# Performance work log

Measured on AMD Instinct MI355X. Metric: run time of the kernel, lower is better.

The kernel has to match this reference:

```python
import jax, jax.numpy as jnp
import numpy as np

P_DIM, L_DIM, D, O = 1100, 1024, 1024, 1024  # protein/label embed dims, latent, mlp width
B, NL = 16, 5000  # num_sequences, num_labels


def setup_inputs() -> dict:
    key = jax.random.key(0)
    ks = jax.random.split(key, 10)
    s = 0.02
    return {
        "sequence_embeddings": jax.random.normal(ks[0], (B, P_DIM), jnp.float32),
        "label_embeddings": jax.random.normal(ks[1], (NL, L_DIM), jnp.float32),
        "Wp": jax.random.normal(ks[2], (D, P_DIM), jnp.float32) * s,  # W_p (no bias)
        "Wl": jax.random.normal(ks[3], (D, L_DIM), jnp.float32) * s,  # W_l (no bias)
        "W1": jax.random.normal(ks[4], (O, 2 * D), jnp.float32) * s,  # Linear(2D -> O)
        "b1": jnp.zeros((O,), jnp.float32),
        "W2": jax.random.normal(ks[5], (O, O), jnp.float32) * s,      # Linear(O -> O)
        "b2": jnp.zeros((O,), jnp.float32),
        "W3": jax.random.normal(ks[6], (1, O), jnp.float32) * s,      # Linear(O -> 1)
        "b3": jnp.zeros((1,), jnp.float32),
    }


def reference(sequence_embeddings, label_embeddings, Wp, Wl, W1, b1, W2, b2, W3, b3):
    # Latent projections
    P_e = sequence_embeddings @ Wp.T           # [B, D]
    L_e = label_embeddings @ Wl.T              # [NL, D]
    # First MLP layer on concat([P_e, L_e]) over the cross join, computed by
    # splitting W1 into its P and L halves and broadcast-summing (same math as
    # cat + Linear, avoids materializing the [B*NL, 2D] concat).
    hp = P_e @ W1[:, :D].T                     # [B, O]
    hl = L_e @ W1[:, D:].T                     # [NL, O]
    h = jax.nn.relu(hp[:, None, :] + hl[None, :, :] + b1)   # [B, NL, O]
    h = jax.nn.relu(h @ W2.T + b2)             # [B, NL, O]
    logits = (h @ W3.T + b3)[..., 0]           # [B, NL]
    return logits
```

## Files before the change

### kernel.cpp

```cpp
#include <hip/hip_runtime.h>
#include <hip/hip_bf16.h>
#include <stdint.h>

typedef __bf16 bf16;
typedef __bf16 bf16x4 __attribute__((ext_vector_type(4)));
typedef __bf16 bf16x8 __attribute__((ext_vector_type(8)));
typedef float floatx4 __attribute__((ext_vector_type(4)));

#define B_SEQ 16
#define NLBL  5000
#define DLAT  1024
#define PDIM  1100
#define NROWS (B_SEQ * NLBL)

__device__ __forceinline__ void gload_lds16(const bf16* g, bf16* l) {
    __builtin_amdgcn_global_load_lds(
        (const __attribute__((address_space(1))) void*)g,
        (__attribute__((address_space(3))) void*)l, 16, 0, 0);
}

__device__ __forceinline__ bf16x8 cvt8(const float* s) {
    floatx4 a = *(const floatx4*)s;
    floatx4 b = *(const floatx4*)(s + 4);
    bf16x8 o;
    o[0] = (bf16)a.x; o[1] = (bf16)a.y; o[2] = (bf16)a.z; o[3] = (bf16)a.w;
    o[4] = (bf16)b.x; o[5] = (bf16)b.y; o[6] = (bf16)b.z; o[7] = (bf16)b.w;
    return o;
}

#define SEG1 2500
#define SEG2 3012
#define SEG3 3524
#define SEG4 4548
#define SEG5 4804
#define SEG6 5117

__global__ __launch_bounds__(256)
void prep_kernel(const float* __restrict__ label, bf16* __restrict__ label_b,
                 const float* __restrict__ W2, bf16* __restrict__ W2_b,
                 const float* __restrict__ W1, bf16* __restrict__ W1l_b,
                 const float* __restrict__ Wl, bf16* __restrict__ WlT_b,
                 const float* __restrict__ seq, const float* __restrict__ Wp,
                 float* __restrict__ Pe,
                 float* __restrict__ out, const float* __restrict__ b3) {
    __shared__ float tile[32][33];
    const int blk = blockIdx.x;
    const int t = threadIdx.x;

    if (blk < SEG1) {
        int i = blk * 256 + t;
        ((bf16x8*)label_b)[i] = cvt8(label + (size_t)i * 8);
    } else if (blk < SEG2) {
        int i = (blk - SEG1) * 256 + t;
        ((bf16x8*)W2_b)[i] = cvt8(W2 + (size_t)i * 8);
    } else if (blk < SEG3) {
        int i = (blk - SEG2) * 256 + t;
        int o = i >> 7, c = (i & 127) * 8;
        ((bf16x8*)W1l_b)[i] = cvt8(W1 + (size_t)o * 2048 + 1024 + c);
    } else if (blk < SEG4) {
        int local = blk - SEG3;
        int bx = (local & 31) * 32, by = (local >> 5) * 32;
        int tx = t & 31, ty = t >> 5;
#pragma unroll
        for (int i = 0; i < 32; i += 8)
            tile[ty + i][tx] = Wl[(size_t)(by + ty + i) * 1024 + bx + tx];
        __syncthreads();
#pragma unroll
        for (int i = 0; i < 32; i += 8)
            WlT_b[(size_t)(bx + ty + i) * 1024 + by + tx] = (bf16)tile[tx][ty + i];
    } else if (blk < SEG5) {
        int w = (blk - SEG4) * 4 + (t >> 6);
        int l = t & 63;
        floatx4 wv[5];
#pragma unroll
        for (int k = 0; k < 5; ++k) {
            int g = l + 64 * k;
            wv[k] = (g < 275) ? *(const floatx4*)(Wp + (size_t)w * PDIM + g * 4)
                              : floatx4{0.f, 0.f, 0.f, 0.f};
        }
        for (int b = 0; b < B_SEQ; ++b) {
            float acc = 0.f;
#pragma unroll
            for (int k = 0; k < 5; ++k) {
                int g = l + 64 * k;
                if (g < 275) {
                    floatx4 sv = *(const floatx4*)(seq + (size_t)b * PDIM + g * 4);
                    acc += wv[k].x * sv.x + wv[k].y * sv.y + wv[k].z * sv.z + wv[k].w * sv.w;
                }
            }
#pragma unroll
            for (int off = 32; off; off >>= 1) acc += __shfl_xor(acc, off, 64);
            if (l == 0) Pe[b * DLAT + w] = acc;
        }
    } else {
        int i = (blk - SEG5) * 256 + t;
        if (i < NROWS) out[i] = b3[0];
    }
}


__global__ __launch_bounds__(256)
void mid_kernel(const float* __restrict__ Pe, const float* __restrict__ W1,
                const float* __restrict__ b1, float* __restrict__ hpb,
                const bf16* __restrict__ A, const bf16* __restrict__ Bt,
                bf16* __restrict__ C) {
    __shared__ bf16 As[64 * 64];
    __shared__ bf16 Bs[64 * 64];
    const int t = threadIdx.x;

    if (blockIdx.x < 256) {
        int w = blockIdx.x * 4 + (t >> 6);
        int l = t & 63;
        floatx4 wv[4];
#pragma unroll
        for (int k = 0; k < 4; ++k)
            wv[k] = *(const floatx4*)(W1 + (size_t)w * 2048 + (l + 64 * k) * 4);
        for (int b = 0; b < B_SEQ; ++b) {
            float acc = 0.f;
#pragma unroll
            for (int k = 0; k < 4; ++k) {
                floatx4 pv = *(const floatx4*)(Pe + (size_t)b * DLAT + (l + 64 * k) * 4);
                acc += wv[k].x * pv.x + wv[k].y * pv.y + wv[k].z * pv.z + wv[k].w * pv.w;
            }
#pragma unroll
            for (int off = 32; off; off >>= 1) acc += __shfl_xor(acc, off, 64);
            if (l == 0) hpb[b * DLAT + w] = acc + b1[w];
        }
        return;
    }

    int idx = blockIdx.x - 256;
    const int n0 = (idx & 15) * 64;
    const int m0 = (idx >> 4) * 64;
    const int wave = t >> 6, lane = t & 63;
    const int wm = (wave & 1) * 32, wn = (wave >> 1) * 32;
    const int lm = lane & 15, quad = lane >> 4;
    const int srow = t >> 2;
    const int sq = t & 3;

    floatx4 acc[2][2] = {};

    for (int k0 = 0; k0 < 1024; k0 += 64) {
#pragma unroll
        for (int p = 0; p < 2; ++p) {
            int cg = (p * 4 + sq) ^ (srow & 7);
            gload_lds16(A + (size_t)(m0 + srow) * 1024 + k0 + cg * 8, As + p * 2048 + (t & 192) * 8);
            gload_lds16(Bt + (size_t)(n0 + srow) * 1024 + k0 + cg * 8, Bs + p * 2048 + (t & 192) * 8);
        }
        __syncthreads();
#pragma unroll
        for (int ks = 0; ks < 2; ++ks) {
            bf16x8 af[2], bg[2];
#pragma unroll
            for (int mi = 0; mi < 2; ++mi) {
                int r = wm + mi * 16 + lm;
                int cg = (ks * 4 + quad) ^ (r & 7);
                af[mi] = *(const bf16x8*)(As + (cg >> 2) * 2048 + r * 32 + (cg & 3) * 8);
            }
#pragma unroll
            for (int ni = 0; ni < 2; ++ni) {
                int r = wn + ni * 16 + lm;
                int cg = (ks * 4 + quad) ^ (r & 7);
                bg[ni] = *(const bf16x8*)(Bs + (cg >> 2) * 2048 + r * 32 + (cg & 3) * 8);
            }
#pragma unroll
            for (int mi = 0; mi < 2; ++mi)
#pragma unroll
                for (int ni = 0; ni < 2; ++ni)
                    acc[mi][ni] = __builtin_amdgcn_mfma_f32_16x16x32_bf16(af[mi], bg[ni], acc[mi][ni], 0, 0, 0);
        }
        __syncthreads();
    }

#pragma unroll
    for (int mi = 0; mi < 2; ++mi)
#pragma unroll
        for (int r = 0; r < 4; ++r)
#pragma unroll
            for (int ni = 0; ni < 2; ++ni) {
                int row = m0 + wm + mi * 16 + quad * 4 + r;
                int col = n0 + wn + ni * 16 + lm;
                C[(size_t)row * 1024 + col] = (bf16)acc[mi][ni][r];
            }
}


__global__ __launch_bounds__(256)
void hl_h1_kernel(const bf16* __restrict__ A, const bf16* __restrict__ Bt,
                  const float* __restrict__ hpb, bf16* __restrict__ h1) {
    __shared__ bf16 As[128 * 64];
    __shared__ bf16 Bs[128 * 64];
    const int t = threadIdx.x;
    const int n0 = blockIdx.x * 128;
    const int m0 = blockIdx.y * 128;
    const int wave = t >> 6, lane = t & 63;
    const int wm = (wave & 1) * 64, wn = (wave >> 1) * 64;
    const int lm = lane & 15, quad = lane >> 4;
    const int sw = lm & 7;
    const int srow = t >> 3;
    const int scg0 = t & 7;
    const int sbase = (t & 192) * 8;

    floatx4 acc[4][4] = {};

    for (int k0 = 0; k0 < 1024; k0 += 64) {
#pragma unroll
        for (int p = 0; p < 4; ++p) {
            int row = p * 32 + srow;
            int cg = scg0 ^ (row & 7);
            int grow = m0 + row; if (grow >= NLBL) grow = NLBL - 1;
            gload_lds16(A + (size_t)grow * 1024 + k0 + cg * 8, As + p * 2048 + sbase);
        }
#pragma unroll
        for (int p = 0; p < 4; ++p) {
            int row = p * 32 + srow;
            int cg = scg0 ^ (row & 7);
            gload_lds16(Bt + (size_t)(n0 + row) * 1024 + k0 + cg * 8, Bs + p * 2048 + sbase);
        }
        __syncthreads();
#pragma unroll
        for (int k = 0; k < 64; k += 32) {
            bf16x8 af[4], bg[4];
            int ko = (((k >> 3) + quad) ^ sw) * 8;
#pragma unroll
            for (int mi = 0; mi < 4; ++mi)
                af[mi] = *(const bf16x8*)(As + (wm + mi * 16 + lm) * 64 + ko);
#pragma unroll
            for (int ni = 0; ni < 4; ++ni)
                bg[ni] = *(const bf16x8*)(Bs + (wn + ni * 16 + lm) * 64 + ko);
#pragma unroll
            for (int mi = 0; mi < 4; ++mi)
#pragma unroll
                for (int ni = 0; ni < 4; ++ni)
                    acc[mi][ni] = __builtin_amdgcn_mfma_f32_16x16x32_bf16(af[mi], bg[ni], acc[mi][ni], 0, 0, 0);
        }
        __syncthreads();
    }

    float* hpbs = (float*)As;
    {
        int dl = (t & 31) * 4;
        int b = t >> 5;
        *(floatx4*)(hpbs + b * 128 + dl) =
            *(const floatx4*)(hpb + (size_t)b * DLAT + n0 + dl);
        *(floatx4*)(hpbs + (b + 8) * 128 + dl) =
            *(const floatx4*)(hpb + (size_t)(b + 8) * DLAT + n0 + dl);
    }
    __syncthreads();

#pragma unroll
    for (int mi = 0; mi < 4; ++mi) {
#pragma unroll
        for (int r = 0; r < 4; ++r) {
            int n = m0 + wm + mi * 16 + quad * 4 + r;
            if (n >= NLBL) continue;
#pragma unroll
            for (int ni = 0; ni < 4; ++ni) {
                int dl = wn + ni * 16 + lm;
                float hlv = acc[mi][ni][r];
                bf16* dst = h1 + (size_t)n * 1024 + n0 + dl;
#pragma unroll
                for (int b = 0; b < B_SEQ; ++b) {
                    float v = fmaxf(hpbs[b * 128 + dl] + hlv, 0.f);
                    dst[(size_t)b * NLBL * 1024] = (bf16)v;
                    dst += 0;
                }
            }
        }
    }
}


__global__ __launch_bounds__(256)
void gemm_h2(const bf16* __restrict__ h1, const bf16* __restrict__ W2b,
             const float* __restrict__ b2, const float* __restrict__ W3,
             float* __restrict__ out) {
    __shared__ bf16 As[128 * 64];
    __shared__ bf16 Bs[128 * 64];
    const int t = threadIdx.x;
    int flat = blockIdx.x;
    int x = flat & 7;
    int s = flat >> 3;
    int mt, nt;
    if (s < 624) { mt = x * 78 + (s >> 3); nt = s & 7; }
    else         { mt = 624; nt = x; }
    const int m0 = mt * 128, n0 = nt * 128;

    const int wave = t >> 6, lane = t & 63;
    const int wm = (wave & 1) * 64, wn = (wave >> 1) * 64;
    const int lm = lane & 15, quad = lane >> 4;
    const int sw = lm & 7;
    const int srow = t >> 3;
    const int scg0 = t & 7;
    const int sbase = (t & 192) * 8;

    floatx4 acc[4][4] = {};
    const bf16* Abase = h1 + (size_t)m0 * 1024;
    const bf16* Bbase = W2b + (size_t)n0 * 1024;

    for (int k0 = 0; k0 < 1024; k0 += 64) {
#pragma unroll
        for (int p = 0; p < 4; ++p) {
            int row = p * 32 + srow;
            int cg = scg0 ^ (row & 7);
            gload_lds16(Abase + (size_t)row * 1024 + k0 + cg * 8, As + p * 2048 + sbase);
        }
#pragma unroll
        for (int p = 0; p < 4; ++p) {
            int row = p * 32 + srow;
            int cg = scg0 ^ (row & 7);
            gload_lds16(Bbase + (size_t)row * 1024 + k0 + cg * 8, Bs + p * 2048 + sbase);
        }
        __syncthreads();
#pragma unroll
        for (int k = 0; k < 64; k += 32) {
            bf16x8 af[4], bg[4];
            int ko = (((k >> 3) + quad) ^ sw) * 8;
#pragma unroll
            for (int mi = 0; mi < 4; ++mi)
                af[mi] = *(const bf16x8*)(As + (wm + mi * 16 + lm) * 64 + ko);
#pragma unroll
            for (int ni = 0; ni < 4; ++ni)
                bg[ni] = *(const bf16x8*)(Bs + (wn + ni * 16 + lm) * 64 + ko);
#pragma unroll
            for (int mi = 0; mi < 4; ++mi)
#pragma unroll
                for (int ni = 0; ni < 4; ++ni)
                    acc[mi][ni] = __builtin_amdgcn_mfma_f32_16x16x32_bf16(af[mi], bg[ni], acc[mi][ni], 0, 0, 0);
        }
        __syncthreads();
    }

    float w3v[4], b2v[4];
#pragma unroll
    for (int ni = 0; ni < 4; ++ni) {
        int col = n0 + wn + ni * 16 + lm;
        w3v[ni] = W3[col];
        b2v[ni] = b2[col];
    }
#pragma unroll
    for (int mi = 0; mi < 4; ++mi) {
#pragma unroll
        for (int r = 0; r < 4; ++r) {
            float sacc = 0.f;
#pragma unroll
            for (int ni = 0; ni < 4; ++ni)
                sacc += fmaxf(acc[mi][ni][r] + b2v[ni], 0.f) * w3v[ni];
            sacc += __shfl_xor(sacc, 1, 64);
            sacc += __shfl_xor(sacc, 2, 64);
            sacc += __shfl_xor(sacc, 4, 64);
            sacc += __shfl_xor(sacc, 8, 64);
            if (lm == 0)
                atomicAdd(out + m0 + wm + mi * 16 + quad * 4 + r, sacc);
        }
    }
}


extern "C" void kernel_launch(void* const* d_in, const int* in_sizes, int n_in,
                              void* d_out, int out_size, void* d_ws, size_t ws_size,
                              hipStream_t stream) {
    const float* seq   = (const float*)d_in[0];
    const float* label = (const float*)d_in[1];
    const float* Wp    = (const float*)d_in[2];
    const float* Wl    = (const float*)d_in[3];
    const float* W1    = (const float*)d_in[4];
    const float* b1    = (const float*)d_in[5];
    const float* W2    = (const float*)d_in[6];
    const float* b2    = (const float*)d_in[7];
    const float* W3    = (const float*)d_in[8];
    const float* b3    = (const float*)d_in[9];
    float* out = (float*)d_out;
    (void)n_in; (void)in_sizes; (void)out_size; (void)ws_size;

    size_t off = 0;
    auto alloc = [&](size_t bytes) {
        void* p = (char*)d_ws + off;
        off += (bytes + 255) & ~(size_t)255;
        return p;
    };
    bf16* label_b = (bf16*)alloc((size_t)NLBL * 1024 * 2);
    bf16* WlT_b   = (bf16*)alloc((size_t)1024 * 1024 * 2);
    bf16* W1l_b   = (bf16*)alloc((size_t)1024 * 1024 * 2);
    bf16* W2_b    = (bf16*)alloc((size_t)1024 * 1024 * 2);
    bf16* M_bf    = (bf16*)alloc((size_t)1024 * 1024 * 2);
    float* Pe     = (float*)alloc((size_t)B_SEQ * 1024 * 4);
    float* hpb    = (float*)alloc((size_t)B_SEQ * 1024 * 4);
    bf16* h1      = (bf16*)alloc((size_t)NROWS * 1024 * 2);

    prep_kernel<<<SEG6, 256, 0, stream>>>(label, label_b, W2, W2_b, W1, W1l_b,
                                          Wl, WlT_b, seq, Wp, Pe, out, b3);
    mid_kernel<<<512, 256, 0, stream>>>(Pe, W1, b1, hpb, W1l_b, WlT_b, M_bf);
    hl_h1_kernel<<<dim3(8, 40), 256, 0, stream>>>(label_b, M_bf, hpb, h1);
    gemm_h2<<<5000, 256, 0, stream>>>(h1, W2_b, b2, W3, out);
}
```

Before: 354.7 us.

## Fuse weight-product GEMM into prep kernel and vectorize h1 epilogue stores

The W1_l·Wl product GEMM now runs inside the prep kernel, reading fp32 W1 and Wl directly, converting to bf16 while staging into padded LDS, and transposing Wl on the fly. This removes the separate bf16 W1l/WlT buffers, their conversion and transpose passes, and one kernel boundary; the hp bias projection moves to its own small kernel. The hl_h1 epilogue now stages the accumulator tile through LDS so each thread writes 16-byte bf16x8 rows of h1 instead of scattered 2-byte stores. The cost is non-async fp32 loads, scalar transposed LDS writes in the fused GEMM, and a larger shared-memory footprint in hl_h1.

```diff
diff --git a/kernel.cpp b/kernel.cpp
--- a/kernel.cpp
+++ b/kernel.cpp
@@ -28,48 +28,82 @@
     return o;
 }
 
-#define SEG1 2500
-#define SEG2 3012
-#define SEG3 3524
-#define SEG4 4548
-#define SEG5 4804
-#define SEG6 5117
+#define PSEG_M    256
+#define PSEG_LAB  2756
+#define PSEG_W2   3268
+#define PSEG_PE   3524
+#define PSEG_END  3837
 
 __global__ __launch_bounds__(256)
 void prep_kernel(const float* __restrict__ label, bf16* __restrict__ label_b,
                  const float* __restrict__ W2, bf16* __restrict__ W2_b,
-                 const float* __restrict__ W1, bf16* __restrict__ W1l_b,
-                 const float* __restrict__ Wl, bf16* __restrict__ WlT_b,
+                 const float* __restrict__ W1, const float* __restrict__ Wl,
+                 bf16* __restrict__ M_bf,
                  const float* __restrict__ seq, const float* __restrict__ Wp,
                  float* __restrict__ Pe,
                  float* __restrict__ out, const float* __restrict__ b3) {
-    __shared__ float tile[32][33];
+    __shared__ bf16 MAs[64 * 72];
+    __shared__ bf16 MBs[64 * 72];
     const int blk = blockIdx.x;
     const int t = threadIdx.x;
 
-    if (blk < SEG1) {
-        int i = blk * 256 + t;
+    if (blk < PSEG_M) {
+        const int m0 = (blk >> 4) * 64;
+        const int n0g = (blk & 15) * 64;
+        const int wave = t >> 6, lane = t & 63;
+        const int wm = (wave & 1) * 32, wn = (wave >> 1) * 32;
+        const int lm = lane & 15, quad = lane >> 4;
+        const int a_r = t >> 2, a_c = (t & 3) * 16;
+        const int b_kr = t >> 4, b_l = (t & 15) * 4;
+        floatx4 acc[2][2] = {};
+
+        for (int k0 = 0; k0 < 1024; k0 += 64) {
+            const float* ap = W1 + (size_t)(m0 + a_r) * 2048 + 1024 + k0 + a_c;
+            *(bf16x8*)(MAs + a_r * 72 + a_c) = cvt8(ap);
+            *(bf16x8*)(MAs + a_r * 72 + a_c + 8) = cvt8(ap + 8);
+#pragma unroll
+            for (int ps = 0; ps < 4; ++ps) {
+                int kr = b_kr + ps * 16;
+                floatx4 v = *(const floatx4*)(Wl + (size_t)(k0 + kr) * 1024 + n0g + b_l);
+                MBs[(b_l + 0) * 72 + kr] = (bf16)v.x;
+                MBs[(b_l + 1) * 72 + kr] = (bf16)v.y;
+                MBs[(b_l + 2) * 72 + kr] = (bf16)v.z;
+                MBs[(b_l + 3) * 72 + kr] = (bf16)v.w;
+            }
+            __syncthreads();
+#pragma unroll
+            for (int ks = 0; ks < 2; ++ks) {
+                bf16x8 af[2], bg[2];
+#pragma unroll
+                for (int mi = 0; mi < 2; ++mi)
+                    af[mi] = *(const bf16x8*)(MAs + (wm + mi * 16 + lm) * 72 + ks * 32 + quad * 8);
+#pragma unroll
+                for (int ni = 0; ni < 2; ++ni)
+                    bg[ni] = *(const bf16x8*)(MBs + (wn + ni * 16 + lm) * 72 + ks * 32 + quad * 8);
+#pragma unroll
+                for (int mi = 0; mi < 2; ++mi)
+#pragma unroll
+                    for (int ni = 0; ni < 2; ++ni)
+                        acc[mi][ni] = __builtin_amdgcn_mfma_f32_16x16x32_bf16(af[mi], bg[ni], acc[mi][ni], 0, 0, 0);
+            }
+            __syncthreads();
+        }
+#pragma unroll
+        for (int mi = 0; mi < 2; ++mi)
+#pragma unroll
+            for (int r = 0; r < 4; ++r)
+#pragma unroll
+                for (int ni = 0; ni < 2; ++ni)
+                    M_bf[(size_t)(m0 + wm + mi * 16 + quad * 4 + r) * 1024 + n0g + wn + ni * 16 + lm] =
+                        (bf16)acc[mi][ni][r];
+    } else if (blk < PSEG_LAB) {
+        int i = (blk - PSEG_M) * 256 + t;
         ((bf16x8*)label_b)[i] = cvt8(label + (size_t)i * 8);
-    } else if (blk < SEG2) {
-        int i = (blk - SEG1) * 256 + t;
+    } else if (blk < PSEG_W2) {
+        int i = (blk - PSEG_LAB) * 256 + t;
         ((bf16x8*)W2_b)[i] = cvt8(W2 + (size_t)i * 8);
-    } else if (blk < SEG3) {
-        int i = (blk - SEG2) * 256 + t;
-        int o = i >> 7, c = (i & 127) * 8;
-        ((bf16x8*)W1l_b)[i] = cvt8(W1 + (size_t)o * 2048 + 1024 + c);
-    } else if (blk < SEG4) {
-        int local = blk - SEG3;
-        int bx = (local & 31) * 32, by = (local >> 5) * 32;
-        int tx = t & 31, ty = t >> 5;
-#pragma unroll
-        for (int i = 0; i < 32; i += 8)
-            tile[ty + i][tx] = Wl[(size_t)(by + ty + i) * 1024 + bx + tx];
-        __syncthreads();
-#pragma unroll
-        for (int i = 0; i < 32; i += 8)
-            WlT_b[(size_t)(bx + ty + i) * 1024 + by + tx] = (bf16)tile[tx][ty + i];
-    } else if (blk < SEG5) {
-        int w = (blk - SEG4) * 4 + (t >> 6);
+    } else if (blk < PSEG_PE) {
+        int w = (blk - PSEG_W2) * 4 + (t >> 6);
         int l = t & 63;
         floatx4 wv[5];
 #pragma unroll
@@ -93,103 +127,44 @@
             if (l == 0) Pe[b * DLAT + w] = acc;
         }
     } else {
-        int i = (blk - SEG5) * 256 + t;
+        int i = (blk - PSEG_PE) * 256 + t;
         if (i < NROWS) out[i] = b3[0];
     }
 }
 
 
 __global__ __launch_bounds__(256)
-void mid_kernel(const float* __restrict__ Pe, const float* __restrict__ W1,
-                const float* __restrict__ b1, float* __restrict__ hpb,
-                const bf16* __restrict__ A, const bf16* __restrict__ Bt,
-                bf16* __restrict__ C) {
-    __shared__ bf16 As[64 * 64];
-    __shared__ bf16 Bs[64 * 64];
-    const int t = threadIdx.x;
-
-    if (blockIdx.x < 256) {
-        int w = blockIdx.x * 4 + (t >> 6);
-        int l = t & 63;
-        floatx4 wv[4];
-#pragma unroll
-        for (int k = 0; k < 4; ++k)
-            wv[k] = *(const floatx4*)(W1 + (size_t)w * 2048 + (l + 64 * k) * 4);
-        for (int b = 0; b < B_SEQ; ++b) {
-            float acc = 0.f;
-#pragma unroll
-            for (int k = 0; k < 4; ++k) {
-                floatx4 pv = *(const floatx4*)(Pe + (size_t)b * DLAT + (l + 64 * k) * 4);
-                acc += wv[k].x * pv.x + wv[k].y * pv.y + wv[k].z * pv.z + wv[k].w * pv.w;
-            }
-#pragma unroll
-            for (int off = 32; off; off >>= 1) acc += __shfl_xor(acc, off, 64);
-            if (l == 0) hpb[b * DLAT + w] = acc + b1[w];
-        }
-        return;
-    }
-
-    int idx = blockIdx.x - 256;
-    const int n0 = (idx & 15) * 64;
-    const int m0 = (idx >> 4) * 64;
-    const int wave = t >> 6, lane = t & 63;
-    const int wm = (wave & 1) * 32, wn = (wave >> 1) * 32;
-    const int lm = lane & 15, quad = lane >> 4;
-    const int srow = t >> 2;
-    const int sq = t & 3;
-
-    floatx4 acc[2][2] = {};
-
-    for (int k0 = 0; k0 < 1024; k0 += 64) {
-#pragma unroll
-        for (int p = 0; p < 2; ++p) {
-            int cg = (p * 4 + sq) ^ (srow & 7);
-            gload_lds16(A + (size_t)(m0 + srow) * 1024 + k0 + cg * 8, As + p * 2048 + (t & 192) * 8);
-            gload_lds16(Bt + (size_t)(n0 + srow) * 1024 + k0 + cg * 8, Bs + p * 2048 + (t & 192) * 8);
-        }
-        __syncthreads();
-#pragma unroll
-        for (int ks = 0; ks < 2; ++ks) {
-            bf16x8 af[2], bg[2];
-#pragma unroll
-            for (int mi = 0; mi < 2; ++mi) {
-                int r = wm + mi * 16 + lm;
-                int cg = (ks * 4 + quad) ^ (r & 7);
-                af[mi] = *(const bf16x8*)(As + (cg >> 2) * 2048 + r * 32 + (cg & 3) * 8);
-            }
-#pragma unroll
-            for (int ni = 0; ni < 2; ++ni) {
-                int r = wn + ni * 16 + lm;
-                int cg = (ks * 4 + quad) ^ (r & 7);
-                bg[ni] = *(const bf16x8*)(Bs + (cg >> 2) * 2048 + r * 32 + (cg & 3) * 8);
-            }
-#pragma unroll
-            for (int mi = 0; mi < 2; ++mi)
-#pragma unroll
-                for (int ni = 0; ni < 2; ++ni)
-                    acc[mi][ni] = __builtin_amdgcn_mfma_f32_16x16x32_bf16(af[mi], bg[ni], acc[mi][ni], 0, 0, 0);
-        }
-        __syncthreads();
-    }
-
-#pragma unroll
-    for (int mi = 0; mi < 2; ++mi)
-#pragma unroll
-        for (int r = 0; r < 4; ++r)
-#pragma unroll
-            for (int ni = 0; ni < 2; ++ni) {
-                int row = m0 + wm + mi * 16 + quad * 4 + r;
-                int col = n0 + wn + ni * 16 + lm;
-                C[(size_t)row * 1024 + col] = (bf16)acc[mi][ni][r];
-            }
+void hpb_kernel(const float* __restrict__ Pe, const float* __restrict__ W1,
+                const float* __restrict__ b1, float* __restrict__ hpb) {
+    int w = blockIdx.x * 4 + (threadIdx.x >> 6);
+    int l = threadIdx.x & 63;
+    floatx4 wv[4];
+#pragma unroll
+    for (int k = 0; k < 4; ++k)
+        wv[k] = *(const floatx4*)(W1 + (size_t)w * 2048 + (l + 64 * k) * 4);
+    for (int b = 0; b < B_SEQ; ++b) {
+        float acc = 0.f;
+#pragma unroll
+        for (int k = 0; k < 4; ++k) {
+            floatx4 pv = *(const floatx4*)(Pe + (size_t)b * DLAT + (l + 64 * k) * 4);
+            acc += wv[k].x * pv.x + wv[k].y * pv.y + wv[k].z * pv.z + wv[k].w * pv.w;
+        }
+#pragma unroll
+        for (int off = 32; off; off >>= 1) acc += __shfl_xor(acc, off, 64);
+        if (l == 0) hpb[b * DLAT + w] = acc + b1[w];
+    }
 }
 
 
 __global__ __launch_bounds__(256)
 void hl_h1_kernel(const bf16* __restrict__ A, const bf16* __restrict__ Bt,
                   const float* __restrict__ hpb, bf16* __restrict__ h1) {
-    __shared__ bf16 As[128 * 64];
-    __shared__ bf16 Bs[128 * 64];
+    __shared__ __align__(16) char smem[43008];
+    bf16* As = (bf16*)smem;
+    bf16* Bs = (bf16*)(smem + 16384);
+    bf16* Ls = (bf16*)smem;
+    float* hpbs = (float*)(smem + 34816);
+
     const int t = threadIdx.x;
     const int n0 = blockIdx.x * 128;
     const int m0 = blockIdx.y * 128;
@@ -237,7 +212,14 @@
         __syncthreads();
     }
 
-    float* hpbs = (float*)As;
+#pragma unroll
+    for (int mi = 0; mi < 4; ++mi)
+#pragma unroll
+        for (int r = 0; r < 4; ++r)
+#pragma unroll
+            for (int ni = 0; ni < 4; ++ni)
+                Ls[(wm + mi * 16 + quad * 4 + r) * 136 + wn + ni * 16 + lm] =
+                    (bf16)acc[mi][ni][r];
     {
         int dl = (t & 31) * 4;
         int b = t >> 5;
@@ -248,24 +230,31 @@
     }
     __syncthreads();
 
-#pragma unroll
-    for (int mi = 0; mi < 4; ++mi) {
-#pragma unroll
-        for (int r = 0; r < 4; ++r) {
-            int n = m0 + wm + mi * 16 + quad * 4 + r;
+    const int g = t & 15;
+    const int r0 = t >> 4;
+    bf16x8 hlv[8];
+#pragma unroll
+    for (int p = 0; p < 8; ++p)
+        hlv[p] = *(const bf16x8*)(Ls + (p * 16 + r0) * 136 + g * 8);
+
+    for (int b = 0; b < B_SEQ; ++b) {
+        floatx4 h0 = *(const floatx4*)(hpbs + b * 128 + g * 8);
+        floatx4 h4 = *(const floatx4*)(hpbs + b * 128 + g * 8 + 4);
+        size_t rowbase = (size_t)b * NLBL * 1024;
+#pragma unroll
+        for (int p = 0; p < 8; ++p) {
+            int n = m0 + p * 16 + r0;
             if (n >= NLBL) continue;
-#pragma unroll
-            for (int ni = 0; ni < 4; ++ni) {
-                int dl = wn + ni * 16 + lm;
-                float hlv = acc[mi][ni][r];
-                bf16* dst = h1 + (size_t)n * 1024 + n0 + dl;
-#pragma unroll
-                for (int b = 0; b < B_SEQ; ++b) {
-                    float v = fmaxf(hpbs[b * 128 + dl] + hlv, 0.f);
-                    dst[(size_t)b * NLBL * 1024] = (bf16)v;
-                    dst += 0;
-                }
-            }
+            bf16x8 o;
+            o[0] = (bf16)fmaxf((float)hlv[p][0] + h0.x, 0.f);
+            o[1] = (bf16)fmaxf((float)hlv[p][1] + h0.y, 0.f);
+            o[2] = (bf16)fmaxf((float)hlv[p][2] + h0.z, 0.f);
+            o[3] = (bf16)fmaxf((float)hlv[p][3] + h0.w, 0.f);
+            o[4] = (bf16)fmaxf((float)hlv[p][4] + h4.x, 0.f);
+            o[5] = (bf16)fmaxf((float)hlv[p][5] + h4.y, 0.f);
+            o[6] = (bf16)fmaxf((float)hlv[p][6] + h4.z, 0.f);
+            o[7] = (bf16)fmaxf((float)hlv[p][7] + h4.w, 0.f);
+            *(bf16x8*)(h1 + rowbase + (size_t)n * 1024 + n0 + g * 8) = o;
         }
     }
 }
@@ -380,17 +369,15 @@
         return p;
     };
     bf16* label_b = (bf16*)alloc((size_t)NLBL * 1024 * 2);
-    bf16* WlT_b   = (bf16*)alloc((size_t)1024 * 1024 * 2);
-    bf16* W1l_b   = (bf16*)alloc((size_t)1024 * 1024 * 2);
     bf16* W2_b    = (bf16*)alloc((size_t)1024 * 1024 * 2);
     bf16* M_bf    = (bf16*)alloc((size_t)1024 * 1024 * 2);
     float* Pe     = (float*)alloc((size_t)B_SEQ * 1024 * 4);
     float* hpb    = (float*)alloc((size_t)B_SEQ * 1024 * 4);
     bf16* h1      = (bf16*)alloc((size_t)NROWS * 1024 * 2);
 
-    prep_kernel<<<SEG6, 256, 0, stream>>>(label, label_b, W2, W2_b, W1, W1l_b,
-                                          Wl, WlT_b, seq, Wp, Pe, out, b3);
-    mid_kernel<<<512, 256, 0, stream>>>(Pe, W1, b1, hpb, W1l_b, WlT_b, M_bf);
+    prep_kernel<<<PSEG_END, 256, 0, stream>>>(label, label_b, W2, W2_b, W1, Wl,
+                                              M_bf, seq, Wp, Pe, out, b3);
+    hpb_kernel<<<256, 256, 0, stream>>>(Pe, W1, b1, hpb);
     hl_h1_kernel<<<dim3(8, 40), 256, 0, stream>>>(label_b, M_bf, hpb, h1);
     gemm_h2<<<5000, 256, 0, stream>>>(h1, W2_b, b2, W3, out);
 }
```

After: 349.8 us. No clear change (-1.4%).
